# Performance work log

Hardware: AMD Instinct MI355X
Metric: run time of the kernel (lower is better)

Reference implementation:

```python
import jax, jax.numpy as jnp
import numpy as np

EMBED_DIM = 4096
LOW_RANK = 512
BATCH = 8192
K_SEL = 128


def setup_inputs() -> dict:
    key = jax.random.key(0)
    k1, k2, k3, k4 = jax.random.split(key, 4)
    base = jax.random.normal(k1, (BATCH, EMBED_DIM), dtype=jnp.float32)
    source = jax.random.normal(k2, (BATCH, EMBED_DIM), dtype=jnp.float32)
    # fast path: only subspaces[0] is used (all examples share the same index set)
    row = jax.random.randint(k3, (1, K_SEL), 0, LOW_RANK)
    subspaces = jnp.broadcast_to(row, (BATCH, K_SEL)).astype(jnp.int64)
    # orthogonal (column-orthonormal) rotation weight, as produced by
    # torch.nn.utils.parametrizations.orthogonal on [embed_dim, low_rank]
    W, _ = jnp.linalg.qr(jax.random.normal(k4, (EMBED_DIM, LOW_RANK), dtype=jnp.float32))
    return {"base": base, "source": source, "subspaces": subspaces, "W": W}


def reference(base, source, subspaces, W):
    # rotated_base / rotated_source: [B, r]
    # diff in rotated space, gather selected subspace columns, project back.
    sel = subspaces[0]                      # [k] shared index set (fast path)
    diff = (source - base) @ W              # [B, r]
    diff_sel = diff[:, sel]                 # [B, k]
    W_sel = W[:, sel]                       # [d, k]
    out = base + diff_sel @ W_sel.T         # [B, d]
    return out.astype(base.dtype)
```

## Files before the change

kernel.cpp:

```cpp
#include <hip/hip_runtime.h>
#include <hip/hip_bf16.h>

typedef __attribute__((ext_vector_type(4))) float  f32x4;
typedef __attribute__((ext_vector_type(8))) short  short8;
typedef unsigned int u32;

#define EMBED 4096
#define LR    512
#define KSEL  128
#define BATCH 8192

__device__ __forceinline__ short f2bf(float x) {
  union { float f; unsigned u; } c; c.f = x;
  unsigned r = c.u + 0x7FFFu + ((c.u >> 16) & 1u);
  return (short)(r >> 16);
}
__device__ __forceinline__ void gload16(const void* g, void* l) {
  __builtin_amdgcn_global_load_lds((const __attribute__((address_space(1))) u32*)g,
                                   (__attribute__((address_space(3))) u32*)l, 16, 0, 0);
}

__global__ __launch_bounds__(256) void pack_w_kernel(
    const float* __restrict__ W, const int* __restrict__ sel,
    short* __restrict__ Wp, short* __restrict__ Wtp) {
  int idx = blockIdx.x * 256 + threadIdx.x;
  int e = idx >> 7;
  int c = idx & 127;
  int r = sel[c];
  short v = f2bf(W[e * LR + r]);
  Wp [(((e >> 3) << 7) + c) * 8 + (e & 7)] = v;
  Wtp[(((c >> 3) << 12) + e) * 8 + (c & 7)] = v;
}

__global__ __launch_bounds__(256, 2) void gemm1_kernel(
    const float* __restrict__ base, const float* __restrict__ src,
    const short* __restrict__ Wp, short* __restrict__ Tp) {
  __shared__ __align__(16) char smem[65536];
  const int t  = threadIdx.x;
  const int w  = t >> 6, l = t & 63;
  const int lr = l & 15, lg = l >> 4;
  const int row0 = blockIdx.x * 16;
  const int srow = t >> 6;
  const int sc   = t & 63;

  #define STAGE(s, b) do {                                                  \
    char* d_ = smem + (b) * 32768 + t * 16;                                 \
    _Pragma("unroll")                                                       \
    for (int i = 0; i < 4; ++i) {                                           \
      const int row = i * 4 + srow;                                         \
      const size_t go = (size_t)(row0 + row) * EMBED + (s) * 256            \
                        + ((sc ^ (row & 7)) << 2);                          \
      gload16(base + go, d_ + i * 4096);                                    \
      gload16(src  + go, d_ + 16384 + i * 4096);                            \
    }                                                                       \
  } while (0)

  const short8* wq = (const short8*)Wp;
  f32x4 acc0 = {0.f, 0.f, 0.f, 0.f}, acc1 = {0.f, 0.f, 0.f, 0.f};

  STAGE(0, 0);
  int b = 0;
  for (int s = 0; s < 16; ++s) {
    __syncthreads();
    const int kc = s * 256;
    short8 bf[16];
    #pragma unroll
    for (int kstep = 0; kstep < 8; ++kstep) {
      const int kg = ((kc + kstep * 32) >> 3) + lg;
      bf[kstep * 2]     = wq[(size_t)kg * 128 + w * 32 + lr];
      bf[kstep * 2 + 1] = wq[(size_t)kg * 128 + w * 32 + 16 + lr];
    }
    if (s < 15) STAGE(s + 1, b ^ 1);
    const char* tb = smem + b * 32768 + lr * 1024;
    #pragma unroll
    for (int kstep = 0; kstep < 8; ++kstep) {
      const int j0 = (kstep * 8 + lg * 2)     ^ (lr & 7);
      const int j1 = (kstep * 8 + lg * 2 + 1) ^ (lr & 7);
      f32x4 b0 = *(const f32x4*)(tb + j0 * 16);
      f32x4 b1 = *(const f32x4*)(tb + j1 * 16);
      f32x4 s0 = *(const f32x4*)(tb + 16384 + j0 * 16);
      f32x4 s1 = *(const f32x4*)(tb + 16384 + j1 * 16);
      union { short8 v; __hip_bfloat162 h[4]; } u;
      u.h[0] = __float22bfloat162_rn(make_float2(s0[0] - b0[0], s0[1] - b0[1]));
      u.h[1] = __float22bfloat162_rn(make_float2(s0[2] - b0[2], s0[3] - b0[3]));
      u.h[2] = __float22bfloat162_rn(make_float2(s1[0] - b1[0], s1[1] - b1[1]));
      u.h[3] = __float22bfloat162_rn(make_float2(s1[2] - b1[2], s1[3] - b1[3]));
      acc0 = __builtin_amdgcn_mfma_f32_16x16x32_bf16(u.v, bf[kstep * 2],     acc0, 0, 0, 0);
      acc1 = __builtin_amdgcn_mfma_f32_16x16x32_bf16(u.v, bf[kstep * 2 + 1], acc1, 0, 0, 0);
    }
    b ^= 1;
  }
  #undef STAGE

  #pragma unroll
  for (int ct = 0; ct < 2; ++ct) {
    f32x4 a = ct ? acc1 : acc0;
    const int kk = w * 32 + ct * 16 + lr;
    short* dst = Tp + (size_t)(((kk >> 3) << 13) + row0 + (lg << 2)) * 8 + (kk & 7);
    #pragma unroll
    for (int r = 0; r < 4; ++r) dst[r * 8] = f2bf(a[r]);
  }
}

__global__ __launch_bounds__(256) void gemm2_kernel(
    const float* __restrict__ base, const short* __restrict__ Tp,
    const short* __restrict__ Wtp, float* __restrict__ out) {
  const int t  = threadIdx.x;
  const int w  = t >> 6, l = t & 63;
  const int lr = l & 15, lg = l >> 4;
  const int mt = blockIdx.x >> 4, nt = blockIdx.x & 15;
  const int row0 = mt * 64;
  const int col0 = nt * 256 + w * 64;

  short8 afr[4][4];
  #pragma unroll
  for (int m = 0; m < 4; ++m)
    #pragma unroll
    for (int ks = 0; ks < 4; ++ks)
      afr[m][ks] = *(const short8*)(Tp + (size_t)(((ks * 4 + lg) << 13) + row0 + m * 16 + lr) * 8);

  f32x4 acc[4][4];
  #pragma unroll
  for (int m = 0; m < 4; ++m)
    #pragma unroll
    for (int nf = 0; nf < 4; ++nf) acc[m][nf] = (f32x4){0.f, 0.f, 0.f, 0.f};

  #pragma unroll
  for (int nf = 0; nf < 4; ++nf) {
    short8 bfr[4];
    #pragma unroll
    for (int ks = 0; ks < 4; ++ks)
      bfr[ks] = *(const short8*)(Wtp + (size_t)(((ks * 4 + lg) << 12) + col0 + nf * 16 + lr) * 8);
    #pragma unroll
    for (int m = 0; m < 4; ++m)
      #pragma unroll
      for (int ks = 0; ks < 4; ++ks)
        acc[m][nf] = __builtin_amdgcn_mfma_f32_16x16x32_bf16(afr[m][ks], bfr[ks], acc[m][nf], 0, 0, 0);
  }

  #pragma unroll
  for (int m = 0; m < 4; ++m)
    #pragma unroll
    for (int r = 0; r < 4; ++r) {
      const size_t row = row0 + m * 16 + lg * 4 + r;
      #pragma unroll
      for (int nf = 0; nf < 4; ++nf) {
        const size_t o = row * EMBED + col0 + nf * 16 + lr;
        float v = base[o] + acc[m][nf][r];
        __builtin_nontemporal_store(v, &out[o]);
      }
    }
}

extern "C" void kernel_launch(void* const* d_in, const int* in_sizes, int n_in,
                              void* d_out, int out_size, void* d_ws, size_t ws_size,
                              hipStream_t stream) {
  const float* base = (const float*)d_in[0];
  const float* src  = (const float*)d_in[1];
  const int*   sub  = (const int*)d_in[2];
  const float* W    = (const float*)d_in[3];
  float* out = (float*)d_out;

  short* Wp  = (short*)d_ws;
  short* Wtp = Wp  + EMBED * KSEL;
  short* Tp  = Wtp + EMBED * KSEL;

  pack_w_kernel<<<EMBED * KSEL / 256, 256, 0, stream>>>(W, sub, Wp, Wtp);
  gemm1_kernel<<<BATCH / 16, 256, 0, stream>>>(base, src, Wp, Tp);
  gemm2_kernel<<<(BATCH / 64) * 16, 256, 0, stream>>>(base, Tp, Wtp, out);
}
```

Measured before the change: 121.8 us.

## Fuse both GEMMs into one kernel, keeping the projected tile in LDS

```diff
diff --git a/kernel.cpp b/kernel.cpp
--- a/kernel.cpp
+++ b/kernel.cpp
@@ -32,10 +32,11 @@
   Wtp[(((c >> 3) << 12) + e) * 8 + (c & 7)] = v;
 }
 
-__global__ __launch_bounds__(256, 2) void gemm1_kernel(
+__global__ __launch_bounds__(256, 2) void fused_kernel(
     const float* __restrict__ base, const float* __restrict__ src,
-    const short* __restrict__ Wp, short* __restrict__ Tp) {
-  __shared__ __align__(16) char smem[65536];
+    const short* __restrict__ Wp, const short* __restrict__ Wtp,
+    float* __restrict__ out) {
+  __shared__ __align__(16) char smem[65536 + 4096];
   const int t  = threadIdx.x;
   const int w  = t >> 6, l = t & 63;
   const int lr = l & 15, lg = l >> 4;
@@ -92,64 +93,53 @@
   }
   #undef STAGE
 
+  short* Tl = (short*)(smem + 65536);
   #pragma unroll
   for (int ct = 0; ct < 2; ++ct) {
     f32x4 a = ct ? acc1 : acc0;
     const int kk = w * 32 + ct * 16 + lr;
-    short* dst = Tp + (size_t)(((kk >> 3) << 13) + row0 + (lg << 2)) * 8 + (kk & 7);
+    short* dst = Tl + ((kk >> 3) * 16 + (lg << 2)) * 8 + (kk & 7);
     #pragma unroll
     for (int r = 0; r < 4; ++r) dst[r * 8] = f2bf(a[r]);
   }
-}
+  __syncthreads();
 
-__global__ __launch_bounds__(256) void gemm2_kernel(
-    const float* __restrict__ base, const short* __restrict__ Tp,
-    const short* __restrict__ Wtp, float* __restrict__ out) {
-  const int t  = threadIdx.x;
-  const int w  = t >> 6, l = t & 63;
-  const int lr = l & 15, lg = l >> 4;
-  const int mt = blockIdx.x >> 4, nt = blockIdx.x & 15;
-  const int row0 = mt * 64;
-  const int col0 = nt * 256 + w * 64;
+  short8 afr[4];
+  #pragma unroll
+  for (int ks = 0; ks < 4; ++ks)
+    afr[ks] = *(const short8*)(Tl + ((ks * 4 + lg) * 16 + lr) * 8);
 
-  short8 afr[4][4];
-  #pragma unroll
-  for (int m = 0; m < 4; ++m)
+  const int colw = w * 1024;
+  #pragma unroll 1
+  for (int nt = 0; nt < 16; ++nt) {
+    const int col0 = colw + nt * 64;
+    short8 bfr[4][4];
     #pragma unroll
-    for (int ks = 0; ks < 4; ++ks)
-      afr[m][ks] = *(const short8*)(Tp + (size_t)(((ks * 4 + lg) << 13) + row0 + m * 16 + lr) * 8);
-
-  f32x4 acc[4][4];
-  #pragma unroll
-  for (int m = 0; m < 4; ++m)
-    #pragma unroll
-    for (int nf = 0; nf < 4; ++nf) acc[m][nf] = (f32x4){0.f, 0.f, 0.f, 0.f};
-
-  #pragma unroll
-  for (int nf = 0; nf < 4; ++nf) {
-    short8 bfr[4];
-    #pragma unroll
-    for (int ks = 0; ks < 4; ++ks)
-      bfr[ks] = *(const short8*)(Wtp + (size_t)(((ks * 4 + lg) << 12) + col0 + nf * 16 + lr) * 8);
-    #pragma unroll
-    for (int m = 0; m < 4; ++m)
+    for (int nf = 0; nf < 4; ++nf)
       #pragma unroll
       for (int ks = 0; ks < 4; ++ks)
-        acc[m][nf] = __builtin_amdgcn_mfma_f32_16x16x32_bf16(afr[m][ks], bfr[ks], acc[m][nf], 0, 0, 0);
-  }
-
-  #pragma unroll
-  for (int m = 0; m < 4; ++m)
+        bfr[nf][ks] = *(const short8*)(Wtp +
+            (size_t)(((ks * 4 + lg) << 12) + col0 + nf * 16 + lr) * 8);
+    f32x4 acc2[4];
+    #pragma unroll
+    for (int nf = 0; nf < 4; ++nf) {
+      acc2[nf] = (f32x4){0.f, 0.f, 0.f, 0.f};
+      #pragma unroll
+      for (int ks = 0; ks < 4; ++ks)
+        acc2[nf] = __builtin_amdgcn_mfma_f32_16x16x32_bf16(afr[ks], bfr[nf][ks],
+                                                           acc2[nf], 0, 0, 0);
+    }
     #pragma unroll
     for (int r = 0; r < 4; ++r) {
-      const size_t row = row0 + m * 16 + lg * 4 + r;
+      const size_t row = row0 + lg * 4 + r;
       #pragma unroll
       for (int nf = 0; nf < 4; ++nf) {
         const size_t o = row * EMBED + col0 + nf * 16 + lr;
-        float v = base[o] + acc[m][nf][r];
+        float v = base[o] + acc2[nf][r];
         __builtin_nontemporal_store(v, &out[o]);
       }
     }
+  }
 }
 
 extern "C" void kernel_launch(void* const* d_in, const int* in_sizes, int n_in,
@@ -162,10 +152,8 @@
   float* out = (float*)d_out;
 
   short* Wp  = (short*)d_ws;
-  short* Wtp = Wp  + EMBED * KSEL;
-  short* Tp  = Wtp + EMBED * KSEL;
+  short* Wtp = Wp + EMBED * KSEL;
 
   pack_w_kernel<<<EMBED * KSEL / 256, 256, 0, stream>>>(W, sub, Wp, Wtp);
-  gemm1_kernel<<<BATCH / 16, 256, 0, stream>>>(base, src, Wp, Tp);
-  gemm2_kernel<<<(BATCH / 64) * 16, 256, 0, stream>>>(base, Tp, Wtp, out);
+  fused_kernel<<<BATCH / 16, 256, 0, stream>>>(base, src, Wp, Wtp, out);
 }
```

After: 126.2 us. 1.04x slower.

## Split first GEMM into separate base and source projections to halve LDS use

Applied to the files above, without the earlier changes.

```diff
diff --git a/kernel.cpp b/kernel.cpp
--- a/kernel.cpp
+++ b/kernel.cpp
@@ -32,10 +32,11 @@
   Wtp[(((c >> 3) << 12) + e) * 8 + (c & 7)] = v;
 }
 
-__global__ __launch_bounds__(256, 2) void gemm1_kernel(
-    const float* __restrict__ base, const float* __restrict__ src,
-    const short* __restrict__ Wp, short* __restrict__ Tp) {
-  __shared__ __align__(16) char smem[65536];
+template<int SUB>
+__global__ __launch_bounds__(256, 4) void gemm1p_kernel(
+    const float* __restrict__ A, const short* __restrict__ Wp,
+    float* __restrict__ Tpa, short* __restrict__ Tp) {
+  __shared__ __align__(16) char smem[32768];
   const int t  = threadIdx.x;
   const int w  = t >> 6, l = t & 63;
   const int lr = l & 15, lg = l >> 4;
@@ -44,14 +45,13 @@
   const int sc   = t & 63;
 
   #define STAGE(s, b) do {                                                  \
-    char* d_ = smem + (b) * 32768 + t * 16;                                 \
+    char* d_ = smem + (b) * 16384 + t * 16;                                 \
     _Pragma("unroll")                                                       \
     for (int i = 0; i < 4; ++i) {                                           \
       const int row = i * 4 + srow;                                         \
       const size_t go = (size_t)(row0 + row) * EMBED + (s) * 256            \
                         + ((sc ^ (row & 7)) << 2);                          \
-      gload16(base + go, d_ + i * 4096);                                    \
-      gload16(src  + go, d_ + 16384 + i * 4096);                            \
+      gload16(A + go, d_ + i * 4096);                                       \
     }                                                                       \
   } while (0)
 
@@ -71,20 +71,18 @@
       bf[kstep * 2 + 1] = wq[(size_t)kg * 128 + w * 32 + 16 + lr];
     }
     if (s < 15) STAGE(s + 1, b ^ 1);
-    const char* tb = smem + b * 32768 + lr * 1024;
+    const char* tb = smem + b * 16384 + lr * 1024;
     #pragma unroll
     for (int kstep = 0; kstep < 8; ++kstep) {
       const int j0 = (kstep * 8 + lg * 2)     ^ (lr & 7);
       const int j1 = (kstep * 8 + lg * 2 + 1) ^ (lr & 7);
-      f32x4 b0 = *(const f32x4*)(tb + j0 * 16);
-      f32x4 b1 = *(const f32x4*)(tb + j1 * 16);
-      f32x4 s0 = *(const f32x4*)(tb + 16384 + j0 * 16);
-      f32x4 s1 = *(const f32x4*)(tb + 16384 + j1 * 16);
+      f32x4 a0 = *(const f32x4*)(tb + j0 * 16);
+      f32x4 a1 = *(const f32x4*)(tb + j1 * 16);
       union { short8 v; __hip_bfloat162 h[4]; } u;
-      u.h[0] = __float22bfloat162_rn(make_float2(s0[0] - b0[0], s0[1] - b0[1]));
-      u.h[1] = __float22bfloat162_rn(make_float2(s0[2] - b0[2], s0[3] - b0[3]));
-      u.h[2] = __float22bfloat162_rn(make_float2(s1[0] - b1[0], s1[1] - b1[1]));
-      u.h[3] = __float22bfloat162_rn(make_float2(s1[2] - b1[2], s1[3] - b1[3]));
+      u.h[0] = __float22bfloat162_rn(make_float2(a0[0], a0[1]));
+      u.h[1] = __float22bfloat162_rn(make_float2(a0[2], a0[3]));
+      u.h[2] = __float22bfloat162_rn(make_float2(a1[0], a1[1]));
+      u.h[3] = __float22bfloat162_rn(make_float2(a1[2], a1[3]));
       acc0 = __builtin_amdgcn_mfma_f32_16x16x32_bf16(u.v, bf[kstep * 2],     acc0, 0, 0, 0);
       acc1 = __builtin_amdgcn_mfma_f32_16x16x32_bf16(u.v, bf[kstep * 2 + 1], acc1, 0, 0, 0);
     }
@@ -96,9 +94,16 @@
   for (int ct = 0; ct < 2; ++ct) {
     f32x4 a = ct ? acc1 : acc0;
     const int kk = w * 32 + ct * 16 + lr;
-    short* dst = Tp + (size_t)(((kk >> 3) << 13) + row0 + (lg << 2)) * 8 + (kk & 7);
-    #pragma unroll
-    for (int r = 0; r < 4; ++r) dst[r * 8] = f2bf(a[r]);
+    if (SUB == 0) {
+      #pragma unroll
+      for (int r = 0; r < 4; ++r)
+        Tpa[(size_t)(row0 + lg * 4 + r) * KSEL + kk] = a[r];
+    } else {
+      short* dst = Tp + (size_t)(((kk >> 3) << 13) + row0 + (lg << 2)) * 8 + (kk & 7);
+      #pragma unroll
+      for (int r = 0; r < 4; ++r)
+        dst[r * 8] = f2bf(a[r] - Tpa[(size_t)(row0 + lg * 4 + r) * KSEL + kk]);
+    }
   }
 }
 
@@ -164,8 +169,10 @@
   short* Wp  = (short*)d_ws;
   short* Wtp = Wp  + EMBED * KSEL;
   short* Tp  = Wtp + EMBED * KSEL;
+  float* Tpa = (float*)(Tp + BATCH * KSEL);
 
   pack_w_kernel<<<EMBED * KSEL / 256, 256, 0, stream>>>(W, sub, Wp, Wtp);
-  gemm1_kernel<<<BATCH / 16, 256, 0, stream>>>(base, src, Wp, Tp);
+  gemm1p_kernel<0><<<BATCH / 16, 256, 0, stream>>>(base, Wp, Tpa, nullptr);
+  gemm1p_kernel<1><<<BATCH / 16, 256, 0, stream>>>(src,  Wp, Tpa, Tp);
   gemm2_kernel<<<(BATCH / 64) * 16, 256, 0, stream>>>(base, Tp, Wtp, out);
 }
```

Result: slower. 162.0 us (+33.0%).
